# Kernel optimization log

Measured on AMD Instinct MI355X. Metric: run time of the kernel, lower is better.

Reference implementation:

```python
import jax, jax.numpy as jnp
import numpy as np

N_FEATURES, D_IN, D_OUT = 64, 128, 128
BATCH = 8192

def setup_inputs() -> dict:
    key = jax.random.key(0)
    kx, kw, kb = jax.random.split(key, 3)
    x = jax.random.normal(kx, (BATCH, N_FEATURES, D_IN), dtype=jnp.float32)
    # mimic nn.Linear init: U(-1/sqrt(d_in), 1/sqrt(d_in)) for weight and bias
    bound = 1.0 / np.sqrt(D_IN)
    weight = jax.random.uniform(kw, (N_FEATURES, D_IN, D_OUT), dtype=jnp.float32, minval=-bound, maxval=bound)
    bias = jax.random.uniform(kb, (N_FEATURES, D_OUT), dtype=jnp.float32, minval=-bound, maxval=bound)
    return {"x": x, "weight": weight, "bias": bias}

def reference(x, weight, bias):
    # per-feature linear: [B,F,I] x [F,I,O] -> [B,F,O]; same math as
    # (x[...,None] * weight[None]).sum(-2) + bias[None], expressed as grouped GEMM
    out = jnp.einsum('bfi,fio->bfo', x, weight)
    return out + bias[None]
```

## Files before the change

### kernel.cpp

```cpp
#include <hip/hip_runtime.h>
#include <hip/hip_bf16.h>


#define NF 64
#define DI 128
#define DO 128
#define WROWS 16
#define BMT (WROWS * 4)
#define TILES 4
#define CHUNKS 32
#define RS (NF * DI)

typedef __attribute__((ext_vector_type(8))) short short8;
typedef __attribute__((ext_vector_type(4))) float floatx4;

static __device__ __forceinline__ unsigned short f2bf(float f) {
    union { float f; unsigned u; } v; v.f = f;
    unsigned r = v.u + 0x7fffu + ((v.u >> 16) & 1u);
    return (unsigned short)(r >> 16);
}

__global__ __launch_bounds__(256, 4)
void nlinear_kernel(const float* __restrict__ x,
                    const float* __restrict__ w,
                    const float* __restrict__ bias,
                    float* __restrict__ out) {
    __shared__ unsigned short lds_wt[DO * DI];
    __shared__ float lds_bias[DO];

    int b = blockIdx.x;
    int logical = (b & 7) * (NF * CHUNKS / 8) + (b >> 3);
    int f = logical >> 5;
    int chunk = logical & 31;

    int tid  = threadIdx.x;
    int lane = tid & 63;
    int wid  = tid >> 6;
    int lrow = lane & 15;
    int kq   = lane >> 4;

    const float* wf = w + (size_t)f * DI * DO;
    #pragma unroll
    for (int it = 0; it < 16; ++it) {
        int id = it * 256 + tid;
        int i  = id >> 5;
        int o4 = (id & 31) << 2;
        floatx4 v = *(const floatx4*)(wf + i * DO + o4);
        #pragma unroll
        for (int j = 0; j < 4; ++j) {
            int o = o4 + j;
            int byte = o * 256 + ((i * 2) ^ ((o & 15) << 4));
            *(unsigned short*)((char*)lds_wt + byte) = f2bf(v[j]);
        }
    }
    if (tid < DO) lds_bias[tid] = bias[f * DO + tid];
    __syncthreads();

    size_t row0 = (size_t)chunk * (BMT * TILES) + wid * WROWS + lrow;
    const float* xw = x   + row0 * RS + f * DI;
    float*       ow = out + row0 * RS + f * DO + kq * 4;

    for (int t = 0; t < TILES; ++t) {
        const float* xp = xw + (size_t)t * BMT * RS;

        floatx4 raw[8];
        #pragma unroll
        for (int kk = 0; kk < 4; ++kk)
            #pragma unroll
            for (int h = 0; h < 2; ++h)
                raw[kk * 2 + h] = *(const floatx4*)(xp + kk * 32 + kq * 8 + h * 4);

        short8 ax[4];
        #pragma unroll
        for (int kk = 0; kk < 4; ++kk) {
            floatx4 v0 = raw[kk * 2], v1 = raw[kk * 2 + 1];
            short8 a;
            a[0] = (short)f2bf(v0[0]); a[1] = (short)f2bf(v0[1]);
            a[2] = (short)f2bf(v0[2]); a[3] = (short)f2bf(v0[3]);
            a[4] = (short)f2bf(v1[0]); a[5] = (short)f2bf(v1[1]);
            a[6] = (short)f2bf(v1[2]); a[7] = (short)f2bf(v1[3]);
            ax[kk] = a;
        }

        floatx4 acc[8];
        #pragma unroll
        for (int n = 0; n < 8; ++n)
            acc[n] = *(const floatx4*)(lds_bias + n * 16 + kq * 4);

        #pragma unroll
        for (int kk = 0; kk < 4; ++kk) {
            int kb = (kk * 64 + kq * 16) ^ (lrow << 4);
            #pragma unroll
            for (int n = 0; n < 8; ++n) {
                short8 bw = *(const short8*)((const char*)lds_wt
                              + (n * 16 + lrow) * 256 + kb);
                acc[n] = __builtin_amdgcn_mfma_f32_16x16x32_bf16(
                             bw, ax[kk], acc[n], 0, 0, 0);
            }
        }

        float* op = ow + (size_t)t * BMT * RS;
        #pragma unroll
        for (int n = 0; n < 8; ++n)
            *(floatx4*)(op + n * 16) = acc[n];
    }
}

extern "C" void kernel_launch(void* const* d_in, const int* in_sizes, int n_in,
                              void* d_out, int out_size, void* d_ws, size_t ws_size,
                              hipStream_t stream) {
    const float* x    = (const float*)d_in[0];
    const float* wght = (const float*)d_in[1];
    const float* bias = (const float*)d_in[2];
    float* out        = (float*)d_out;

    dim3 grid(NF * CHUNKS);
    dim3 block(256);
    nlinear_kernel<<<grid, block, 0, stream>>>(x, wght, bias, out);
}
```

Measured before the change: 181.5 us.

## Double-buffer x tile loads and enlarge blocks to 512 threads with fewer blocks

Measured after the change: 358.7 us. +97.6%, slower.

```diff
diff --git a/kernel.cpp b/kernel.cpp
--- a/kernel.cpp
+++ b/kernel.cpp
@@ -6,9 +6,10 @@
 #define DI 128
 #define DO 128
 #define WROWS 16
-#define BMT (WROWS * 4)
-#define TILES 4
-#define CHUNKS 32
+#define WAVES 8
+#define BMT (WROWS * WAVES)
+#define TILES 8
+#define ROWSPB (BMT * TILES)
 #define RS (NF * DI)
 
 typedef __attribute__((ext_vector_type(8))) short short8;
@@ -20,7 +21,7 @@
     return (unsigned short)(r >> 16);
 }
 
-__global__ __launch_bounds__(256, 4)
+__global__ __launch_bounds__(512, 4)
 void nlinear_kernel(const float* __restrict__ x,
                     const float* __restrict__ w,
                     const float* __restrict__ bias,
@@ -29,10 +30,8 @@
     __shared__ float lds_bias[DO];
 
     int b = blockIdx.x;
-    int logical = (b & 7) * (NF * CHUNKS / 8) + (b >> 3);
-    int f = logical >> 5;
-    int chunk = logical & 31;
-
+    int f = b & 63;
+    int q = b >> 6;
     int tid  = threadIdx.x;
     int lane = tid & 63;
     int wid  = tid >> 6;
@@ -41,8 +40,8 @@
 
     const float* wf = w + (size_t)f * DI * DO;
     #pragma unroll
-    for (int it = 0; it < 16; ++it) {
-        int id = it * 256 + tid;
+    for (int it = 0; it < 8; ++it) {
+        int id = it * 512 + tid;
         int i  = id >> 5;
         int o4 = (id & 31) << 2;
         floatx4 v = *(const floatx4*)(wf + i * DO + o4);
@@ -56,54 +55,60 @@
     if (tid < DO) lds_bias[tid] = bias[f * DO + tid];
     __syncthreads();
 
-    size_t row0 = (size_t)chunk * (BMT * TILES) + wid * WROWS + lrow;
-    const float* xw = x   + row0 * RS + f * DI;
+    size_t row0 = (size_t)q * ROWSPB + wid * WROWS + lrow;
+    const float* xw = x   + row0 * RS + f * DI + kq * 8;
     float*       ow = out + row0 * RS + f * DO + kq * 4;
 
-    for (int t = 0; t < TILES; ++t) {
-        const float* xp = xw + (size_t)t * BMT * RS;
+    floatx4 rawA[8], rawB[8];
 
-        floatx4 raw[8];
+    auto load_tile = [&](floatx4* r, int t) {
+        const float* p = xw + (size_t)t * BMT * RS;
         #pragma unroll
         for (int kk = 0; kk < 4; ++kk)
             #pragma unroll
             for (int h = 0; h < 2; ++h)
-                raw[kk * 2 + h] = *(const floatx4*)(xp + kk * 32 + kq * 8 + h * 4);
+                r[kk * 2 + h] = *(const floatx4*)(p + kk * 32 + h * 4);
+    };
 
-        short8 ax[4];
+    auto compute_store = [&](const floatx4* r, int t) {
+        floatx4 acc[8];
+        #pragma unroll
+        for (int n = 0; n < 8; ++n)
+            acc[n] = *(const floatx4*)(lds_bias + n * 16 + kq * 4);
         #pragma unroll
         for (int kk = 0; kk < 4; ++kk) {
-            floatx4 v0 = raw[kk * 2], v1 = raw[kk * 2 + 1];
+            floatx4 v0 = r[kk * 2], v1 = r[kk * 2 + 1];
             short8 a;
             a[0] = (short)f2bf(v0[0]); a[1] = (short)f2bf(v0[1]);
             a[2] = (short)f2bf(v0[2]); a[3] = (short)f2bf(v0[3]);
             a[4] = (short)f2bf(v1[0]); a[5] = (short)f2bf(v1[1]);
             a[6] = (short)f2bf(v1[2]); a[7] = (short)f2bf(v1[3]);
-            ax[kk] = a;
-        }
-
-        floatx4 acc[8];
-        #pragma unroll
-        for (int n = 0; n < 8; ++n)
-            acc[n] = *(const floatx4*)(lds_bias + n * 16 + kq * 4);
-
-        #pragma unroll
-        for (int kk = 0; kk < 4; ++kk) {
             int kb = (kk * 64 + kq * 16) ^ (lrow << 4);
             #pragma unroll
             for (int n = 0; n < 8; ++n) {
                 short8 bw = *(const short8*)((const char*)lds_wt
                               + (n * 16 + lrow) * 256 + kb);
                 acc[n] = __builtin_amdgcn_mfma_f32_16x16x32_bf16(
-                             bw, ax[kk], acc[n], 0, 0, 0);
+                             bw, a, acc[n], 0, 0, 0);
             }
         }
-
         float* op = ow + (size_t)t * BMT * RS;
         #pragma unroll
         for (int n = 0; n < 8; ++n)
             *(floatx4*)(op + n * 16) = acc[n];
+    };
+
+    load_tile(rawA, 0);
+    load_tile(rawB, 1);
+    #pragma unroll 1
+    for (int t = 0; t < TILES - 2; t += 2) {
+        compute_store(rawA, t);
+        load_tile(rawA, t + 2);
+        compute_store(rawB, t + 1);
+        if (t + 3 < TILES) load_tile(rawB, t + 3);
     }
+    compute_store(rawA, TILES - 2);
+    compute_store(rawB, TILES - 1);
 }
 
 extern "C" void kernel_launch(void* const* d_in, const int* in_sizes, int n_in,
@@ -114,7 +119,7 @@
     const float* bias = (const float*)d_in[2];
     float* out        = (float*)d_out;
 
-    dim3 grid(NF * CHUNKS);
-    dim3 block(256);
+    dim3 grid(NF * 8);
+    dim3 block(512);
     nlinear_kernel<<<grid, block, 0, stream>>>(x, wght, bias, out);
 }
```

## Prefetch next x tile into registers with inline-asm loads and explicit waitcnt

Applied to the files above, without the earlier changes.

After: 160.1 us. 11.8% less time.

```diff
diff --git a/kernel.cpp b/kernel.cpp
--- a/kernel.cpp
+++ b/kernel.cpp
@@ -6,9 +6,11 @@
 #define DI 128
 #define DO 128
 #define WROWS 16
-#define BMT (WROWS * 4)
-#define TILES 4
-#define CHUNKS 32
+#define WAVES 4
+#define BMT (WROWS * WAVES)
+#define TILES 8
+#define ROWSPB (BMT * TILES)
+#define CHUNKS 16
 #define RS (NF * DI)
 
 typedef __attribute__((ext_vector_type(8))) short short8;
@@ -20,6 +22,20 @@
     return (unsigned short)(r >> 16);
 }
 
+#define ISSUE8(r, p)                                                     \
+    asm volatile(                                                        \
+        "global_load_dwordx4 %0, %8, off\n\t"                            \
+        "global_load_dwordx4 %1, %8, off offset:16\n\t"                  \
+        "global_load_dwordx4 %2, %8, off offset:128\n\t"                 \
+        "global_load_dwordx4 %3, %8, off offset:144\n\t"                 \
+        "global_load_dwordx4 %4, %8, off offset:256\n\t"                 \
+        "global_load_dwordx4 %5, %8, off offset:272\n\t"                 \
+        "global_load_dwordx4 %6, %8, off offset:384\n\t"                 \
+        "global_load_dwordx4 %7, %8, off offset:400\n\t"                 \
+        : "=&v"(r[0]), "=&v"(r[1]), "=&v"(r[2]), "=&v"(r[3]),            \
+          "=&v"(r[4]), "=&v"(r[5]), "=&v"(r[6]), "=&v"(r[7])             \
+        : "v"(p) : "memory")
+
 __global__ __launch_bounds__(256, 4)
 void nlinear_kernel(const float* __restrict__ x,
                     const float* __restrict__ w,
@@ -30,8 +46,8 @@
 
     int b = blockIdx.x;
     int logical = (b & 7) * (NF * CHUNKS / 8) + (b >> 3);
-    int f = logical >> 5;
-    int chunk = logical & 31;
+    int f = logical >> 4;
+    int chunk = logical & 15;
 
     int tid  = threadIdx.x;
     int lane = tid & 63;
@@ -39,54 +55,51 @@
     int lrow = lane & 15;
     int kq   = lane >> 4;
 
+    size_t row0 = (size_t)chunk * ROWSPB + wid * WROWS + lrow;
+    const float* xw = x   + row0 * RS + f * DI + kq * 8;
+    float*       ow = out + row0 * RS + f * DO + kq * 4;
+
+    floatx4 raw[8];
+    ISSUE8(raw, xw);
+
     const float* wf = w + (size_t)f * DI * DO;
     #pragma unroll
-    for (int it = 0; it < 16; ++it) {
+    for (int it = 0; it < 8; ++it) {
         int id = it * 256 + tid;
-        int i  = id >> 5;
         int o4 = (id & 31) << 2;
-        floatx4 v = *(const floatx4*)(wf + i * DO + o4);
+        int i  = (id >> 5) * 2;
+        floatx4 v0 = *(const floatx4*)(wf + i * DO + o4);
+        floatx4 v1 = *(const floatx4*)(wf + (i + 1) * DO + o4);
         #pragma unroll
         for (int j = 0; j < 4; ++j) {
             int o = o4 + j;
             int byte = o * 256 + ((i * 2) ^ ((o & 15) << 4));
-            *(unsigned short*)((char*)lds_wt + byte) = f2bf(v[j]);
+            unsigned pk = (unsigned)f2bf(v0[j]) | ((unsigned)f2bf(v1[j]) << 16);
+            *(unsigned*)((char*)lds_wt + byte) = pk;
         }
     }
     if (tid < DO) lds_bias[tid] = bias[f * DO + tid];
     __syncthreads();
 
-    size_t row0 = (size_t)chunk * (BMT * TILES) + wid * WROWS + lrow;
-    const float* xw = x   + row0 * RS + f * DI;
-    float*       ow = out + row0 * RS + f * DO + kq * 4;
+    short8 ax[4];
+    #pragma unroll
+    for (int kk = 0; kk < 4; ++kk) {
+        floatx4 v0 = raw[kk * 2], v1 = raw[kk * 2 + 1];
+        short8 a;
+        a[0] = (short)f2bf(v0[0]); a[1] = (short)f2bf(v0[1]);
+        a[2] = (short)f2bf(v0[2]); a[3] = (short)f2bf(v0[3]);
+        a[4] = (short)f2bf(v1[0]); a[5] = (short)f2bf(v1[1]);
+        a[6] = (short)f2bf(v1[2]); a[7] = (short)f2bf(v1[3]);
+        ax[kk] = a;
+    }
+    ISSUE8(raw, xw + (size_t)BMT * RS);
 
+    #pragma unroll
     for (int t = 0; t < TILES; ++t) {
-        const float* xp = xw + (size_t)t * BMT * RS;
-
-        floatx4 raw[8];
-        #pragma unroll
-        for (int kk = 0; kk < 4; ++kk)
-            #pragma unroll
-            for (int h = 0; h < 2; ++h)
-                raw[kk * 2 + h] = *(const floatx4*)(xp + kk * 32 + kq * 8 + h * 4);
-
-        short8 ax[4];
-        #pragma unroll
-        for (int kk = 0; kk < 4; ++kk) {
-            floatx4 v0 = raw[kk * 2], v1 = raw[kk * 2 + 1];
-            short8 a;
-            a[0] = (short)f2bf(v0[0]); a[1] = (short)f2bf(v0[1]);
-            a[2] = (short)f2bf(v0[2]); a[3] = (short)f2bf(v0[3]);
-            a[4] = (short)f2bf(v1[0]); a[5] = (short)f2bf(v1[1]);
-            a[6] = (short)f2bf(v1[2]); a[7] = (short)f2bf(v1[3]);
-            ax[kk] = a;
-        }
-
         floatx4 acc[8];
         #pragma unroll
         for (int n = 0; n < 8; ++n)
             acc[n] = *(const floatx4*)(lds_bias + n * 16 + kq * 4);
-
         #pragma unroll
         for (int kk = 0; kk < 4; ++kk) {
             int kb = (kk * 64 + kq * 16) ^ (lrow << 4);
@@ -98,11 +111,27 @@
                              bw, ax[kk], acc[n], 0, 0, 0);
             }
         }
-
         float* op = ow + (size_t)t * BMT * RS;
         #pragma unroll
         for (int n = 0; n < 8; ++n)
             *(floatx4*)(op + n * 16) = acc[n];
+
+        if (t < TILES - 1) {
+            asm volatile("s_waitcnt vmcnt(8)" ::: "memory");
+            __builtin_amdgcn_sched_barrier(0);
+            #pragma unroll
+            for (int kk = 0; kk < 4; ++kk) {
+                floatx4 v0 = raw[kk * 2], v1 = raw[kk * 2 + 1];
+                short8 a;
+                a[0] = (short)f2bf(v0[0]); a[1] = (short)f2bf(v0[1]);
+                a[2] = (short)f2bf(v0[2]); a[3] = (short)f2bf(v0[3]);
+                a[4] = (short)f2bf(v1[0]); a[5] = (short)f2bf(v1[1]);
+                a[6] = (short)f2bf(v1[2]); a[7] = (short)f2bf(v1[3]);
+                ax[kk] = a;
+            }
+            if (t < TILES - 2)
+                ISSUE8(raw, xw + (size_t)(t + 2) * BMT * RS);
+        }
     }
 }
 
```

## Group four features per block and register-prefetch next x tile via inline asm

Applied to the files above, without the earlier changes.

Measured after the change: 186.3 us. 1.03x slower.

```diff
diff --git a/kernel.cpp b/kernel.cpp
--- a/kernel.cpp
+++ b/kernel.cpp
@@ -5,10 +5,12 @@
 #define NF 64
 #define DI 128
 #define DO 128
-#define WROWS 16
-#define BMT (WROWS * 4)
+#define G 4
+#define FG 16
+#define CHUNKS 16
+#define ROWSPB 512
+#define BMT 128
 #define TILES 4
-#define CHUNKS 32
 #define RS (NF * DI)
 
 typedef __attribute__((ext_vector_type(8))) short short8;
@@ -19,19 +21,68 @@
     unsigned r = v.u + 0x7fffu + ((v.u >> 16) & 1u);
     return (unsigned short)(r >> 16);
 }
-
-__global__ __launch_bounds__(256, 4)
+static __device__ __forceinline__ float bflo(unsigned u) {
+    union { unsigned u; float f; } v; v.u = u << 16; return v.f;
+}
+static __device__ __forceinline__ float bfhi(unsigned u) {
+    union { unsigned u; float f; } v; v.u = u & 0xffff0000u; return v.f;
+}
+
+#define ISSUE32(r, p)                                                     \
+    asm volatile(                                                         \
+        "global_load_dwordx4 %0, %32, off\n\t"                            \
+        "global_load_dwordx4 %1, %32, off offset:16\n\t"                  \
+        "global_load_dwordx4 %2, %32, off offset:128\n\t"                 \
+        "global_load_dwordx4 %3, %32, off offset:144\n\t"                 \
+        "global_load_dwordx4 %4, %32, off offset:256\n\t"                 \
+        "global_load_dwordx4 %5, %32, off offset:272\n\t"                 \
+        "global_load_dwordx4 %6, %32, off offset:384\n\t"                 \
+        "global_load_dwordx4 %7, %32, off offset:400\n\t"                 \
+        "global_load_dwordx4 %8, %32, off offset:512\n\t"                 \
+        "global_load_dwordx4 %9, %32, off offset:528\n\t"                 \
+        "global_load_dwordx4 %10, %32, off offset:640\n\t"                \
+        "global_load_dwordx4 %11, %32, off offset:656\n\t"                \
+        "global_load_dwordx4 %12, %32, off offset:768\n\t"                \
+        "global_load_dwordx4 %13, %32, off offset:784\n\t"                \
+        "global_load_dwordx4 %14, %32, off offset:896\n\t"                \
+        "global_load_dwordx4 %15, %32, off offset:912\n\t"                \
+        "global_load_dwordx4 %16, %32, off offset:1024\n\t"               \
+        "global_load_dwordx4 %17, %32, off offset:1040\n\t"               \
+        "global_load_dwordx4 %18, %32, off offset:1152\n\t"               \
+        "global_load_dwordx4 %19, %32, off offset:1168\n\t"               \
+        "global_load_dwordx4 %20, %32, off offset:1280\n\t"               \
+        "global_load_dwordx4 %21, %32, off offset:1296\n\t"               \
+        "global_load_dwordx4 %22, %32, off offset:1408\n\t"               \
+        "global_load_dwordx4 %23, %32, off offset:1424\n\t"               \
+        "global_load_dwordx4 %24, %32, off offset:1536\n\t"               \
+        "global_load_dwordx4 %25, %32, off offset:1552\n\t"               \
+        "global_load_dwordx4 %26, %32, off offset:1664\n\t"               \
+        "global_load_dwordx4 %27, %32, off offset:1680\n\t"               \
+        "global_load_dwordx4 %28, %32, off offset:1792\n\t"               \
+        "global_load_dwordx4 %29, %32, off offset:1808\n\t"               \
+        "global_load_dwordx4 %30, %32, off offset:1920\n\t"               \
+        "global_load_dwordx4 %31, %32, off offset:1936\n\t"               \
+        : "=&v"(r[0]), "=&v"(r[1]), "=&v"(r[2]), "=&v"(r[3]),             \
+          "=&v"(r[4]), "=&v"(r[5]), "=&v"(r[6]), "=&v"(r[7]),             \
+          "=&v"(r[8]), "=&v"(r[9]), "=&v"(r[10]), "=&v"(r[11]),           \
+          "=&v"(r[12]), "=&v"(r[13]), "=&v"(r[14]), "=&v"(r[15]),         \
+          "=&v"(r[16]), "=&v"(r[17]), "=&v"(r[18]), "=&v"(r[19]),         \
+          "=&v"(r[20]), "=&v"(r[21]), "=&v"(r[22]), "=&v"(r[23]),         \
+          "=&v"(r[24]), "=&v"(r[25]), "=&v"(r[26]), "=&v"(r[27]),         \
+          "=&v"(r[28]), "=&v"(r[29]), "=&v"(r[30]), "=&v"(r[31])          \
+        : "v"(p) : "memory")
+
+__global__ __launch_bounds__(512, 2)
 void nlinear_kernel(const float* __restrict__ x,
                     const float* __restrict__ w,
                     const float* __restrict__ bias,
                     float* __restrict__ out) {
-    __shared__ unsigned short lds_wt[DO * DI];
-    __shared__ float lds_bias[DO];
+    __shared__ unsigned short lds_wt[G * DI * DO];
 
     int b = blockIdx.x;
-    int logical = (b & 7) * (NF * CHUNKS / 8) + (b >> 3);
-    int f = logical >> 5;
-    int chunk = logical & 31;
+    int fg    = b >> 4;
+    int chunk = b & 15;
+    int g0 = fg * G;
 
     int tid  = threadIdx.x;
     int lane = tid & 63;
@@ -39,70 +90,101 @@
     int lrow = lane & 15;
     int kq   = lane >> 4;
 
-    const float* wf = w + (size_t)f * DI * DO;
+    unsigned bpk[G][8][2];
+    {
+        const float* bp = bias + (size_t)g0 * DO + kq * 4;
+        #pragma unroll
+        for (int fi = 0; fi < G; ++fi)
+            #pragma unroll
+            for (int n = 0; n < 8; ++n) {
+                floatx4 v = *(const floatx4*)(bp + fi * DO + n * 16);
+                bpk[fi][n][0] = (unsigned)f2bf(v[0]) | ((unsigned)f2bf(v[1]) << 16);
+                bpk[fi][n][1] = (unsigned)f2bf(v[2]) | ((unsigned)f2bf(v[3]) << 16);
+            }
+    }
+
+    size_t row0 = (size_t)chunk * ROWSPB + wid * 16 + lrow;
+    const float* xw = x   + row0 * RS + g0 * DI + kq * 8;
+    float*       ow = out + row0 * RS + g0 * DO + kq * 4;
+
+    floatx4 raw[32];
+    ISSUE32(raw, xw);
+
     #pragma unroll
-    for (int it = 0; it < 16; ++it) {
-        int id = it * 256 + tid;
-        int i  = id >> 5;
-        int o4 = (id & 31) << 2;
-        floatx4 v = *(const floatx4*)(wf + i * DO + o4);
+    for (int fi = 0; fi < G; ++fi) {
+        const float* wf = w + (size_t)(g0 + fi) * DI * DO;
+        unsigned short* wt = lds_wt + fi * DI * DO;
         #pragma unroll
-        for (int j = 0; j < 4; ++j) {
-            int o = o4 + j;
-            int byte = o * 256 + ((i * 2) ^ ((o & 15) << 4));
-            *(unsigned short*)((char*)lds_wt + byte) = f2bf(v[j]);
+        for (int it = 0; it < 4; ++it) {
+            int id = it * 512 + tid;
+            int o4 = (id & 31) << 2;
+            int i  = (id >> 5) * 2;
+            floatx4 v0 = *(const floatx4*)(wf + i * DO + o4);
+            floatx4 v1 = *(const floatx4*)(wf + (i + 1) * DO + o4);
+            #pragma unroll
+            for (int j = 0; j < 4; ++j) {
+                int o = o4 + j;
+                int byte = o * 256 + ((i * 2) ^ ((o & 15) << 4));
+                unsigned pk = (unsigned)f2bf(v0[j]) | ((unsigned)f2bf(v1[j]) << 16);
+                *(unsigned*)((char*)wt + byte) = pk;
+            }
         }
     }
-    if (tid < DO) lds_bias[tid] = bias[f * DO + tid];
     __syncthreads();
-
-    size_t row0 = (size_t)chunk * (BMT * TILES) + wid * WROWS + lrow;
-    const float* xw = x   + row0 * RS + f * DI;
-    float*       ow = out + row0 * RS + f * DO + kq * 4;
-
+    asm volatile("s_waitcnt vmcnt(0)" ::: "memory");
+    __builtin_amdgcn_sched_barrier(0);
+
+    #pragma unroll 1
     for (int t = 0; t < TILES; ++t) {
-        const float* xp = xw + (size_t)t * BMT * RS;
-
-        floatx4 raw[8];
+        const float* xnext = xw + (size_t)(t + 1) * BMT * RS;
+        float* op = ow + (size_t)t * BMT * RS;
+
         #pragma unroll
-        for (int kk = 0; kk < 4; ++kk)
-            #pragma unroll
-            for (int h = 0; h < 2; ++h)
-                raw[kk * 2 + h] = *(const floatx4*)(xp + kk * 32 + kq * 8 + h * 4);
-
-        short8 ax[4];
-        #pragma unroll
-        for (int kk = 0; kk < 4; ++kk) {
-            floatx4 v0 = raw[kk * 2], v1 = raw[kk * 2 + 1];
-            short8 a;
-            a[0] = (short)f2bf(v0[0]); a[1] = (short)f2bf(v0[1]);
-            a[2] = (short)f2bf(v0[2]); a[3] = (short)f2bf(v0[3]);
-            a[4] = (short)f2bf(v1[0]); a[5] = (short)f2bf(v1[1]);
-            a[6] = (short)f2bf(v1[2]); a[7] = (short)f2bf(v1[3]);
-            ax[kk] = a;
+        for (int fi = 0; fi < G; ++fi) {
+            asm volatile("s_waitcnt vmcnt(32)" ::: "memory");
+            __builtin_amdgcn_sched_barrier(0);
+
+            short8 ax[4];
+            #pragma unroll
+            for (int kk = 0; kk < 4; ++kk) {
+                floatx4 v0 = raw[fi * 8 + kk * 2];
+                floatx4 v1 = raw[fi * 8 + kk * 2 + 1];
+                short8 a;
+                a[0] = (short)f2bf(v0[0]); a[1] = (short)f2bf(v0[1]);
+                a[2] = (short)f2bf(v0[2]); a[3] = (short)f2bf(v0[3]);
+                a[4] = (short)f2bf(v1[0]); a[5] = (short)f2bf(v1[1]);
+                a[6] = (short)f2bf(v1[2]); a[7] = (short)f2bf(v1[3]);
+                ax[kk] = a;
+            }
+
+            if (fi == G - 1 && t < TILES - 1)
+                ISSUE32(raw, xnext);
+
+            floatx4 acc[8];
+            #pragma unroll
+            for (int n = 0; n < 8; ++n) {
+                acc[n][0] = bflo(bpk[fi][n][0]);
+                acc[n][1] = bfhi(bpk[fi][n][0]);
+                acc[n][2] = bflo(bpk[fi][n][1]);
+                acc[n][3] = bfhi(bpk[fi][n][1]);
+            }
+
+            const char* wtb = (const char*)lds_wt + fi * 32768;
+            #pragma unroll
+            for (int kk = 0; kk < 4; ++kk) {
+                int kb = (kk * 64 + kq * 16) ^ (lrow << 4);
+                #pragma unroll
+                for (int n = 0; n < 8; ++n) {
+                    short8 bw = *(const short8*)(wtb + (n * 16 + lrow) * 256 + kb);
+                    acc[n] = __builtin_amdgcn_mfma_f32_16x16x32_bf16(
+                                 bw, ax[kk], acc[n], 0, 0, 0);
+                }
+            }
+
+            #pragma unroll
+            for (int n = 0; n < 8; ++n)
+                *(floatx4*)(op + fi * DO + n * 16) = acc[n];
         }
-
-        floatx4 acc[8];
-        #pragma unroll
-        for (int n = 0; n < 8; ++n)
-            acc[n] = *(const floatx4*)(lds_bias + n * 16 + kq * 4);
-
-        #pragma unroll
-        for (int kk = 0; kk < 4; ++kk) {
-            int kb = (kk * 64 + kq * 16) ^ (lrow << 4);
-            #pragma unroll
-            for (int n = 0; n < 8; ++n) {
-                short8 bw = *(const short8*)((const char*)lds_wt
-                              + (n * 16 + lrow) * 256 + kb);
-                acc[n] = __builtin_amdgcn_mfma_f32_16x16x32_bf16(
-                             bw, ax[kk], acc[n], 0, 0, 0);
-            }
-        }
-
-        float* op = ow + (size_t)t * BMT * RS;
-        #pragma unroll
-        for (int n = 0; n < 8; ++n)
-            *(floatx4*)(op + n * 16) = acc[n];
     }
 }
 
@@ -114,7 +196,7 @@
     const float* bias = (const float*)d_in[2];
     float* out        = (float*)d_out;
 
-    dim3 grid(NF * CHUNKS);
-    dim3 block(256);
+    dim3 grid(FG * CHUNKS);
+    dim3 block(512);
     nlinear_kernel<<<grid, block, 0, stream>>>(x, wght, bias, out);
 }
```
